# Performance work log

Measured on AMD Instinct MI355X. Metric: run time of the kernel, lower is better.

Reference implementation:

```python
import jax, jax.numpy as jnp
import numpy as np

B, S, N = 1, 128, 256
D_MSA, D_PAIR, D_HID = 256, 128, 32
EPS = 1e-3
LN_EPS = 1e-5


def _layer_norm(x, w, b):
    mu = jnp.mean(x, axis=-1, keepdims=True)
    var = jnp.mean(jnp.square(x - mu), axis=-1, keepdims=True)
    return (x - mu) * jax.lax.rsqrt(var + LN_EPS) * w + b


def setup_inputs() -> dict:
    key = jax.random.key(0)
    ks = jax.random.split(key, 8)
    sc = lambda fan_in: (1.0 / fan_in) ** 0.5
    return {
        "m": jax.random.normal(ks[0], (B, S, N, D_MSA), dtype=jnp.float32),
        "mask": jnp.ones((B, S, N), dtype=jnp.float32),
        "ln_w": jnp.ones((D_MSA,), dtype=jnp.float32),
        "ln_b": jnp.zeros((D_MSA,), dtype=jnp.float32),
        "w1": jax.random.normal(ks[1], (D_HID, D_MSA), dtype=jnp.float32) * sc(D_MSA),
        "b1": jnp.zeros((D_HID,), dtype=jnp.float32),
        "w2": jax.random.normal(ks[2], (D_HID, D_MSA), dtype=jnp.float32) * sc(D_MSA),
        "b2": jnp.zeros((D_HID,), dtype=jnp.float32),
        "w_out": jax.random.normal(ks[3], (D_PAIR, D_HID * D_HID), dtype=jnp.float32) * sc(D_HID * D_HID),
        "b_out": jnp.zeros((D_PAIR,), dtype=jnp.float32),
        "ln_out_w": jnp.ones((D_PAIR,), dtype=jnp.float32),
        "ln_out_b": jnp.zeros((D_PAIR,), dtype=jnp.float32),
        "wz": jax.random.normal(ks[4], (D_PAIR, D_PAIR), dtype=jnp.float32) * sc(D_PAIR),
        "bz": jnp.zeros((D_PAIR,), dtype=jnp.float32),
    }


def reference(m, mask, ln_w, ln_b, w1, b1, w2, b2, w_out, b_out, ln_out_w, ln_out_b, wz, bz):
    # m: [B, S, N, d_msa], mask: [B, S, N]
    x = _layer_norm(m, ln_w, ln_b)
    n_res = mask.shape[-1]
    mk = mask[..., None] * (n_res ** -0.5)          # [B, S, N, 1] (layer_norm_out branch)
    a = (jnp.einsum('bsnd,hd->bsnh', x, w1) + b1) * mk
    b_ = (jnp.einsum('bsnd,hd->bsnh', x, w2) + b2) * mk
    a = jnp.swapaxes(a, -2, -3)                      # [B, N, S, h]
    b_ = jnp.swapaxes(b_, -2, -3)                    # [B, N, S, h]
    outer = jnp.einsum('bisc,bjse->bijce', a, b_)    # [B, N, N, h, h]
    outer = outer.reshape(outer.shape[:-2] + (-1,))  # [B, N, N, h*h]
    z = jnp.einsum('bijk,pk->bijp', outer, w_out) + b_out  # [B, N, N, d_pair]
    norm = jnp.einsum('bsi,bsj->bij', mk[..., 0], mk[..., 0])[..., None]
    z = z / (EPS + norm)
    z = jax.nn.gelu(z, approximate=False)
    z = _layer_norm(z, ln_out_w, ln_out_b)
    z = jnp.einsum('bijp,qp->bijq', z, wz) + bz
    return z
```

## Files before the change

### kernel.cpp

```cpp
#include <hip/hip_runtime.h>
#include <hip/hip_bf16.h>
#include <math.h>

#define EPSC 1e-3f

typedef __attribute__((ext_vector_type(8)))  short  short8;
typedef __attribute__((ext_vector_type(4)))  float  float4v;
typedef __attribute__((ext_vector_type(16))) float  float16v;

static __device__ __forceinline__ unsigned short f2bf(float f) {
    union { float f; unsigned u; } x; x.f = f;
    unsigned r = x.u + 0x7FFFu + ((x.u >> 16) & 1u);
    return (unsigned short)(r >> 16);
}
static __device__ __forceinline__ unsigned pk_bf16(float lo, float hi) {
    union { __hip_bfloat162 h; unsigned u; } cv;
    cv.h = __float22bfloat162_rn(make_float2(lo, hi));
    return cv.u;
}
static __device__ __forceinline__ float4v mfma16(short8 a, short8 b, float4v c) {
    return __builtin_amdgcn_mfma_f32_16x16x32_bf16(a, b, c, 0, 0, 0);
}
static __device__ __forceinline__ float16v mfma32(short8 a, short8 b, float16v c) {
    return __builtin_amdgcn_mfma_f32_32x32x16_bf16(a, b, c, 0, 0, 0);
}

#define OFF_NORM 0ull
#define OFF_AT   262144ull
#define OFF_BT   2359296ull
#define OFF_WOF  4456448ull
#define OFF_WZF  4718592ull
#define OFF_W12  4751360ull

__global__ __launch_bounds__(256) void k_pre(
    const float* __restrict__ m, const float* __restrict__ mask,
    const float* __restrict__ ln_w, const float* __restrict__ ln_b,
    const float* __restrict__ w1, const float* __restrict__ b1,
    const float* __restrict__ w2, const float* __restrict__ b2,
    const float* __restrict__ w_out, const float* __restrict__ wz,
    unsigned short* __restrict__ aT, unsigned short* __restrict__ bT,
    unsigned short* __restrict__ wobF, unsigned short* __restrict__ wzF,
    const unsigned short* __restrict__ w12F_in,
    unsigned short* __restrict__ w12F,
    float* __restrict__ normw)
{
    __shared__ unsigned short xs[64 * 264];
    __shared__ unsigned short tr[64 * 76];
    __shared__ float mkl[64];
    __shared__ float b12[64];
    int t = threadIdx.x;
    int b = blockIdx.x;

    if (b >= 1152) {
        int i = b - 1152, j = t;
        float acc = 0.f;
#pragma unroll 8
        for (int s = 0; s < 128; ++s)
            acc += mask[s * 256 + i] * mask[s * 256 + j];
        normw[i * 256 + j] = acc * (1.0f / 256.0f);
        return;
    }
    if (b >= 512) {
        int idx = (b - 512) * 256 + t;
        if (idx < 131072) {
            int j = idx & 7, lane = (idx >> 3) & 63, k16 = (idx >> 9) & 63, pw = idx >> 15;
            int p = pw * 32 + (lane & 31);
            int k = k16 * 16 + (lane >> 5) * 8 + j;
            wobF[idx] = f2bf(w_out[p * 1024 + k]);
        } else if (idx < 147456) {
            int q = idx - 131072;
            int j = q & 7, lane = (q >> 3) & 63, kk = (q >> 9) & 3, w = q >> 11;
            int p = w * 16 + (lane & 15);
            int k = kk * 32 + (lane >> 4) * 8 + j;
            wzF[q] = f2bf(wz[p * 128 + k]);
        } else if (idx < 163840) {
            int q = idx - 147456;
            int j = q & 7, lane = (q >> 3) & 63, ht = (q >> 9) & 3, kk = q >> 11;
            int h = ht * 16 + (lane & 15);
            int d = kk * 32 + (lane >> 4) * 8 + j;
            w12F[q] = f2bf(h < 32 ? w1[h * 256 + d] : w2[(h - 32) * 256 + d]);
        }
        return;
    }

    int w = t >> 6, lane = t & 63;
    int g = lane >> 4, l15 = lane & 15;
    int n0 = (b & 31) * 8, s0 = (b >> 5) * 8;

    if (t < 64) {
        b12[t] = (t < 32) ? b1[t] : b2[t - 32];
        mkl[t] = mask[(s0 + (t >> 3)) * 256 + n0 + (t & 7)] * 0.0625f;
    }

    float4 lwv = *(const float4*)(ln_w + lane * 4);
    float4 lbv = *(const float4*)(ln_b + lane * 4);

#pragma unroll 4
    for (int i = 0; i < 16; ++i) {
        int r = w * 16 + i;
        size_t gr = (size_t)(s0 + (r >> 3)) * 256 + n0 + (r & 7);
        float4 v = *(const float4*)(m + gr * 256 + lane * 4);
        float sum = v.x + v.y + v.z + v.w;
        float sq = v.x * v.x + v.y * v.y + v.z * v.z + v.w * v.w;
#pragma unroll
        for (int off = 32; off > 0; off >>= 1) {
            sum += __shfl_xor(sum, off, 64);
            sq  += __shfl_xor(sq, off, 64);
        }
        float mu = sum * (1.f / 256.f);
        float rstd = rsqrtf(sq * (1.f / 256.f) - mu * mu + 1e-5f);
        uint2 u;
        u.x = pk_bf16((v.x - mu) * rstd * lwv.x + lbv.x, (v.y - mu) * rstd * lwv.y + lbv.y);
        u.y = pk_bf16((v.z - mu) * rstd * lwv.z + lbv.z, (v.w - mu) * rstd * lwv.w + lbv.w);
        *(uint2*)(xs + r * 264 + lane * 4) = u;
    }
    __syncthreads();

    float4v zf4 = {0.f, 0.f, 0.f, 0.f};
    float4v acc[4]; acc[0] = zf4; acc[1] = zf4; acc[2] = zf4; acc[3] = zf4;
#pragma unroll
    for (int kk = 0; kk < 8; ++kk) {
        short8 af = *(const short8*)(xs + (w * 16 + l15) * 264 + kk * 32 + g * 8);
#pragma unroll
        for (int ht = 0; ht < 4; ++ht) {
            short8 bfr = *(const short8*)(w12F_in + ((size_t)(kk * 4 + ht) * 64 + lane) * 8);
            acc[ht] = mfma16(af, bfr, acc[ht]);
        }
    }
#pragma unroll
    for (int ht = 0; ht < 4; ++ht) {
        int h = ht * 16 + l15;
        float bias = b12[h];
        int rbase = w * 16 + g * 4;
        uint2 u;
        u.x = pk_bf16((acc[ht][0] + bias) * mkl[rbase + 0], (acc[ht][1] + bias) * mkl[rbase + 1]);
        u.y = pk_bf16((acc[ht][2] + bias) * mkl[rbase + 2], (acc[ht][3] + bias) * mkl[rbase + 3]);
        *(uint2*)(tr + h * 76 + rbase) = u;
    }
    __syncthreads();

#pragma unroll
    for (int it = 0; it < 2; ++it) {
        int q = t + it * 256;
        int h = q >> 3, n_l = q & 7;
        unsigned short vv[8];
#pragma unroll
        for (int s_l = 0; s_l < 8; ++s_l)
            vv[s_l] = tr[h * 76 + s_l * 8 + n_l];
        uint4 u;
        u.x = (unsigned)vv[0] | ((unsigned)vv[1] << 16);
        u.y = (unsigned)vv[2] | ((unsigned)vv[3] << 16);
        u.z = (unsigned)vv[4] | ((unsigned)vv[5] << 16);
        u.w = (unsigned)vv[6] | ((unsigned)vv[7] << 16);
        unsigned short* dst = ((h < 32) ? aT : bT) + ((size_t)(n0 + n_l) * 32 + (h & 31)) * 128 + s0;
        *(uint4*)dst = u;
    }
}

__global__ __launch_bounds__(512, 2) void k2_fused(
    const unsigned short* __restrict__ aT, const unsigned short* __restrict__ bT,
    const unsigned short* __restrict__ wobF, const unsigned short* __restrict__ wzF,
    const float* __restrict__ b_out, const float* __restrict__ normw,
    const float* __restrict__ ln_ow, const float* __restrict__ ln_ob,
    const float* __restrict__ bz, float* __restrict__ out)
{
    __shared__ char smem[131072];
    unsigned* s32 = (unsigned*)smem;
    unsigned* oL = (unsigned*)smem;
    float* zL = (float*)smem;
    unsigned short* lnL = (unsigned short*)(smem + 36864);

    int t = threadIdx.x;
    int w = t >> 6, lane = t & 63;
    int g = lane >> 4, l15 = lane & 15;
    int bj = blockIdx.x, bi = blockIdx.y;
    int wn = w & 1, wm = w >> 1;

    {
        const uint4* Agv = (const uint4*)(aT + (size_t)bi * 256 * 128);
        const uint4* Bgv = (const uint4*)(bT + (size_t)bj * 256 * 128);
#pragma unroll
        for (int it = 0; it < 8; ++it) {
            int q = t + it * 512;
            int row = q >> 4, col4 = (q & 15) * 4;
            int dcol = col4 ^ ((row & 7) << 2);
            *(uint4*)(s32 + row * 64 + dcol) = Agv[q];
            *(uint4*)(s32 + 16384 + row * 64 + dcol) = Bgv[q];
        }
    }
    __syncthreads();

    float4v zf4 = {0.f, 0.f, 0.f, 0.f};
    float4v acc[4][8];
#pragma unroll
    for (int fm = 0; fm < 4; ++fm)
#pragma unroll
        for (int fn = 0; fn < 8; ++fn) acc[fm][fn] = zf4;

    {
        int sw = (l15 & 7) << 2;
#pragma unroll
        for (int kk = 0; kk < 4; ++kk) {
            int col = (kk * 16 + g * 4) ^ sw;
            short8 af[4], bf[8];
#pragma unroll
            for (int fm = 0; fm < 4; ++fm) {
                int row = wm * 64 + fm * 16 + l15;
                af[fm] = *(const short8*)((const char*)(s32 + row * 64 + col));
            }
#pragma unroll
            for (int fn = 0; fn < 8; ++fn) {
                int row = wn * 128 + fn * 16 + l15;
                bf[fn] = *(const short8*)((const char*)(s32 + 16384 + row * 64 + col));
            }
#pragma unroll
            for (int fm = 0; fm < 4; ++fm)
#pragma unroll
                for (int fn = 0; fn < 8; ++fn)
                    acc[fm][fn] = mfma16(bf[fn], af[fm], acc[fm][fn]);
        }
    }
    __syncthreads();

#pragma unroll
    for (int fm = 0; fm < 4; ++fm) {
#pragma unroll
        for (int fn = 0; fn < 8; ++fn) {
            int pair = (wm * 2 + (fm >> 1)) * 8 + wn * 4 + (fn >> 1);
            int c = (fm & 1) * 16 + l15;
            int o = (fn & 1) * 8 + 2 * g;
            int off = c * 16 + o;
            int dw = pair * 512 + (off ^ ((((pair & 7) ^ (off >> 6)) & 7) << 2));
            float4v a4 = acc[fm][fn];
            uint2 u;
            u.x = pk_bf16(a4[0], a4[1]);
            u.y = pk_bf16(a4[2], a4[3]);
            *(uint2*)(oL + dw) = u;
        }
    }
    __syncthreads();

    {
        int pw = w & 3, ph = w >> 2;
        int l31 = lane & 31, h2 = lane >> 5;
        int pairR = ph * 32 + l31;
        int prebase = pairR * 512;
        int psw = (pairR & 7);
        float16v acc32 = {0.f};
        const unsigned short* wbase = wobF + (size_t)pw * 32768;
#pragma unroll 8
        for (int k16 = 0; k16 < 64; ++k16) {
            int off = k16 * 8 + h2 * 4;
            int dw = prebase + (off ^ (((psw ^ (off >> 6)) & 7) << 2));
            short8 a2 = *(const short8*)((const char*)(oL + dw));
            short8 b2 = *(const short8*)(wbase + ((size_t)(k16 * 64 + lane)) * 8);
            acc32 = mfma32(a2, b2, acc32);
        }
        __syncthreads();
#pragma unroll
        for (int reg = 0; reg < 16; ++reg) {
            int prow = ph * 32 + (reg & 3) + 8 * (reg >> 2) + 4 * h2;
            zL[prow * 132 + pw * 32 + l31] = acc32[reg];
        }
    }
    __syncthreads();

    {
        const float4 loA = *(const float4*)(ln_ow + l15 * 8);
        const float4 loB = *(const float4*)(ln_ow + l15 * 8 + 4);
        const float4 lbA = *(const float4*)(ln_ob + l15 * 8);
        const float4 lbB = *(const float4*)(ln_ob + l15 * 8 + 4);
        const float4 boA = *(const float4*)(b_out + l15 * 8);
        const float4 boB = *(const float4*)(b_out + l15 * 8 + 4);
        float lw8[8] = {loA.x, loA.y, loA.z, loA.w, loB.x, loB.y, loB.z, loB.w};
        float lb8[8] = {lbA.x, lbA.y, lbA.z, lbA.w, lbB.x, lbB.y, lbB.z, lbB.w};
        float bo8[8] = {boA.x, boA.y, boA.z, boA.w, boB.x, boB.y, boB.z, boB.w};
#pragma unroll
        for (int it = 0; it < 2; ++it) {
            int pair = w * 8 + it * 4 + g;
            int iG = bi * 8 + (pair >> 3), jG = bj * 8 + (pair & 7);
            float inv = 1.0f / (EPSC + normw[iG * 256 + jG]);
            float4v z0 = *(const float4v*)(zL + pair * 132 + l15 * 8);
            float4v z1 = *(const float4v*)(zL + pair * 132 + l15 * 8 + 4);
            float vals[8];
            float sum = 0.f, sq = 0.f;
#pragma unroll
            for (int e2 = 0; e2 < 8; ++e2) {
                float v = ((e2 < 4) ? z0[e2] : z1[e2 - 4]) + bo8[e2];
                v *= inv;
                v = 0.5f * v * (1.0f + erff(v * 0.70710678118654752f));
                vals[e2] = v; sum += v; sq += v * v;
            }
#pragma unroll
            for (int mm = 1; mm <= 8; mm <<= 1) {
                sum += __shfl_xor(sum, mm);
                sq  += __shfl_xor(sq, mm);
            }
            float mu = sum * (1.0f / 128.0f);
            float rstd = rsqrtf(sq * (1.0f / 128.0f) - mu * mu + 1e-5f);
            uint4 upk;
            upk.x = pk_bf16((vals[0] - mu) * rstd * lw8[0] + lb8[0],
                            (vals[1] - mu) * rstd * lw8[1] + lb8[1]);
            upk.y = pk_bf16((vals[2] - mu) * rstd * lw8[2] + lb8[2],
                            (vals[3] - mu) * rstd * lw8[3] + lb8[3]);
            upk.z = pk_bf16((vals[4] - mu) * rstd * lw8[4] + lb8[4],
                            (vals[5] - mu) * rstd * lw8[5] + lb8[5]);
            upk.w = pk_bf16((vals[6] - mu) * rstd * lw8[6] + lb8[6],
                            (vals[7] - mu) * rstd * lw8[7] + lb8[7]);
            *(uint4*)(lnL + pair * 136 + l15 * 8) = upk;
        }
    }
    __syncthreads();

    {
        float4v acc3[4]; acc3[0] = zf4; acc3[1] = zf4; acc3[2] = zf4; acc3[3] = zf4;
#pragma unroll
        for (int kk = 0; kk < 4; ++kk) {
            short8 bfw = *(const short8*)(wzF + ((size_t)(w * 4 + kk) * 64 + lane) * 8);
#pragma unroll
            for (int fr = 0; fr < 4; ++fr) {
                short8 af3 = *(const short8*)(lnL + (fr * 16 + l15) * 136 + kk * 32 + g * 8);
                acc3[fr] = mfma16(af3, bfw, acc3[fr]);
            }
        }
        float bzq = bz[w * 16 + l15];
#pragma unroll
        for (int fr = 0; fr < 4; ++fr) {
#pragma unroll
            for (int r = 0; r < 4; ++r) {
                int pair = fr * 16 + g * 4 + r;
                int row = (bi * 8 + (pair >> 3)) * 256 + bj * 8 + (pair & 7);
                out[(size_t)row * 128 + w * 16 + l15] = acc3[fr][r] + bzq;
            }
        }
    }
}

extern "C" void kernel_launch(void* const* d_in, const int* in_sizes, int n_in,
                              void* d_out, int out_size, void* d_ws, size_t ws_size,
                              hipStream_t stream) {
    const float* m      = (const float*)d_in[0];
    const float* mask   = (const float*)d_in[1];
    const float* ln_w   = (const float*)d_in[2];
    const float* ln_b   = (const float*)d_in[3];
    const float* w1     = (const float*)d_in[4];
    const float* b1     = (const float*)d_in[5];
    const float* w2     = (const float*)d_in[6];
    const float* b2     = (const float*)d_in[7];
    const float* w_out  = (const float*)d_in[8];
    const float* b_out  = (const float*)d_in[9];
    const float* ln_ow  = (const float*)d_in[10];
    const float* ln_ob  = (const float*)d_in[11];
    const float* wz     = (const float*)d_in[12];
    const float* bz     = (const float*)d_in[13];
    float* out = (float*)d_out;
    char*  ws  = (char*)d_ws;

    float* normw          = (float*)(ws + OFF_NORM);
    unsigned short* aTb   = (unsigned short*)(ws + OFF_AT);
    unsigned short* bTb   = (unsigned short*)(ws + OFF_BT);
    unsigned short* wobF  = (unsigned short*)(ws + OFF_WOF);
    unsigned short* wzF   = (unsigned short*)(ws + OFF_WZF);
    unsigned short* w12F  = (unsigned short*)(ws + OFF_W12);

    {
        struct L {
            static __global__ void __launch_bounds__(256) cvt12(
                const float* __restrict__ w1, const float* __restrict__ w2,
                unsigned short* __restrict__ w12F) {
                int q = blockIdx.x * 256 + threadIdx.x;
                int j = q & 7, lane = (q >> 3) & 63, ht = (q >> 9) & 3, kk = q >> 11;
                int h = ht * 16 + (lane & 15);
                int d = kk * 32 + (lane >> 4) * 8 + j;
                w12F[q] = f2bf(h < 32 ? w1[h * 256 + d] : w2[(h - 32) * 256 + d]);
            }
        };
        L::cvt12<<<dim3(64), dim3(256), 0, stream>>>(w1, w2, w12F);
    }
    k_pre<<<dim3(1408), dim3(256), 0, stream>>>(m, mask, ln_w, ln_b, w1, b1, w2, b2,
                                                w_out, wz, aTb, bTb, wobF, wzF,
                                                w12F, w12F, normw);
    k2_fused<<<dim3(32, 32), dim3(512), 0, stream>>>(aTb, bTb, wobF, wzF, b_out, normw,
                                                     ln_ow, ln_ob, bz, out);
}
```

Measured before the change: 166.9 us.

## Split K in the w_out projection, pre-swizzle aT/bT, and widen LayerNorm row loads

In the fused pair kernel, each warp now computes two 32-row output tiles over half of K and shares each w_out fragment between them. The two K-halves go to separate LDS buffers and are summed during the GELU/LayerNorm epilogue, which halves weight-fragment global loads per MFMA. The pre-kernel now writes aT/bT already in the XOR-swizzled tile layout, so the fused kernel copies them into LDS linearly. The MSA LayerNorm now reads four rows per warp pass with a 16-lane reduction, and the xs row pitch is padded to 266. The cost is more LDS for the split accumulators and an extra add in the epilogue.

```diff
diff --git a/kernel.cpp b/kernel.cpp
--- a/kernel.cpp
+++ b/kernel.cpp
@@ -44,7 +44,7 @@
     unsigned short* __restrict__ w12F,
     float* __restrict__ normw)
 {
-    __shared__ unsigned short xs[64 * 264];
+    __shared__ unsigned short xs[64 * 266];
     __shared__ unsigned short tr[64 * 76];
     __shared__ float mkl[64];
     __shared__ float b12[64];
@@ -63,9 +63,10 @@
     if (b >= 512) {
         int idx = (b - 512) * 256 + t;
         if (idx < 131072) {
-            int j = idx & 7, lane = (idx >> 3) & 63, k16 = (idx >> 9) & 63, pw = idx >> 15;
+            int j = idx & 7, lane = (idx >> 3) & 63, k16 = (idx >> 9) & 31;
+            int kh = (idx >> 14) & 1, pw = (idx >> 15) & 3;
             int p = pw * 32 + (lane & 31);
-            int k = k16 * 16 + (lane >> 5) * 8 + j;
+            int k = kh * 512 + k16 * 16 + (lane >> 5) * 8 + j;
             wobF[idx] = f2bf(w_out[p * 1024 + k]);
         } else if (idx < 147456) {
             int q = idx - 131072;
@@ -85,6 +86,7 @@
 
     int w = t >> 6, lane = t & 63;
     int g = lane >> 4, l15 = lane & 15;
+    int rr = lane >> 4, l16 = lane & 15;
     int n0 = (b & 31) * 8, s0 = (b >> 5) * 8;
 
     if (t < 64) {
@@ -92,27 +94,43 @@
         mkl[t] = mask[(s0 + (t >> 3)) * 256 + n0 + (t & 7)] * 0.0625f;
     }
 
-    float4 lwv = *(const float4*)(ln_w + lane * 4);
-    float4 lbv = *(const float4*)(ln_b + lane * 4);
-
-#pragma unroll 4
-    for (int i = 0; i < 16; ++i) {
-        int r = w * 16 + i;
-        size_t gr = (size_t)(s0 + (r >> 3)) * 256 + n0 + (r & 7);
-        float4 v = *(const float4*)(m + gr * 256 + lane * 4);
-        float sum = v.x + v.y + v.z + v.w;
-        float sq = v.x * v.x + v.y * v.y + v.z * v.z + v.w * v.w;
-#pragma unroll
-        for (int off = 32; off > 0; off >>= 1) {
-            sum += __shfl_xor(sum, off, 64);
-            sq  += __shfl_xor(sq, off, 64);
+    float4 lw4[4], lb4[4];
+#pragma unroll
+    for (int q = 0; q < 4; ++q) {
+        lw4[q] = *(const float4*)(ln_w + q * 64 + l16 * 4);
+        lb4[q] = *(const float4*)(ln_b + q * 64 + l16 * 4);
+    }
+
+#pragma unroll
+    for (int pass = 0; pass < 4; ++pass) {
+        int r = w * 16 + pass * 4 + rr;
+        const float* src = m + ((size_t)(s0 + (r >> 3)) * 256 + n0 + (r & 7)) * 256;
+        float4 v[4];
+#pragma unroll
+        for (int q = 0; q < 4; ++q)
+            v[q] = *(const float4*)(src + q * 64 + l16 * 4);
+        float sum = 0.f, sq = 0.f;
+#pragma unroll
+        for (int q = 0; q < 4; ++q) {
+            sum += v[q].x + v[q].y + v[q].z + v[q].w;
+            sq  += v[q].x * v[q].x + v[q].y * v[q].y + v[q].z * v[q].z + v[q].w * v[q].w;
+        }
+#pragma unroll
+        for (int mm = 1; mm <= 8; mm <<= 1) {
+            sum += __shfl_xor(sum, mm);
+            sq  += __shfl_xor(sq, mm);
         }
         float mu = sum * (1.f / 256.f);
         float rstd = rsqrtf(sq * (1.f / 256.f) - mu * mu + 1e-5f);
-        uint2 u;
-        u.x = pk_bf16((v.x - mu) * rstd * lwv.x + lbv.x, (v.y - mu) * rstd * lwv.y + lbv.y);
-        u.y = pk_bf16((v.z - mu) * rstd * lwv.z + lbv.z, (v.w - mu) * rstd * lwv.w + lbv.w);
-        *(uint2*)(xs + r * 264 + lane * 4) = u;
+#pragma unroll
+        for (int q = 0; q < 4; ++q) {
+            uint2 u;
+            u.x = pk_bf16((v[q].x - mu) * rstd * lw4[q].x + lb4[q].x,
+                          (v[q].y - mu) * rstd * lw4[q].y + lb4[q].y);
+            u.y = pk_bf16((v[q].z - mu) * rstd * lw4[q].z + lb4[q].z,
+                          (v[q].w - mu) * rstd * lw4[q].w + lb4[q].w);
+            *(uint2*)(xs + r * 266 + q * 64 + l16 * 4) = u;
+        }
     }
     __syncthreads();
 
@@ -120,7 +138,7 @@
     float4v acc[4]; acc[0] = zf4; acc[1] = zf4; acc[2] = zf4; acc[3] = zf4;
 #pragma unroll
     for (int kk = 0; kk < 8; ++kk) {
-        short8 af = *(const short8*)(xs + (w * 16 + l15) * 264 + kk * 32 + g * 8);
+        short8 af = *(const short8*)(xs + (w * 16 + l15) * 266 + kk * 32 + g * 8);
 #pragma unroll
         for (int ht = 0; ht < 4; ++ht) {
             short8 bfr = *(const short8*)(w12F_in + ((size_t)(kk * 4 + ht) * 64 + lane) * 8);
@@ -152,7 +170,10 @@
         u.y = (unsigned)vv[2] | ((unsigned)vv[3] << 16);
         u.z = (unsigned)vv[4] | ((unsigned)vv[5] << 16);
         u.w = (unsigned)vv[6] | ((unsigned)vv[7] << 16);
-        unsigned short* dst = ((h < 32) ? aT : bT) + ((size_t)(n0 + n_l) * 32 + (h & 31)) * 128 + s0;
+        int row = n_l * 32 + (h & 31);
+        int dwcol = (s0 >> 1) ^ ((row & 7) << 2);
+        unsigned short* dst = ((h < 32) ? aT : bT)
+            + (size_t)(n0 >> 3) * 32768 + row * 128 + dwcol * 2;
         *(uint4*)dst = u;
     }
 }
@@ -167,8 +188,9 @@
     __shared__ char smem[131072];
     unsigned* s32 = (unsigned*)smem;
     unsigned* oL = (unsigned*)smem;
-    float* zL = (float*)smem;
-    unsigned short* lnL = (unsigned short*)(smem + 36864);
+    float* zA = (float*)smem;
+    float* zB = (float*)(smem + 33792);
+    unsigned short* lnL = (unsigned short*)(smem + 67584);
 
     int t = threadIdx.x;
     int w = t >> 6, lane = t & 63;
@@ -177,15 +199,13 @@
     int wn = w & 1, wm = w >> 1;
 
     {
-        const uint4* Agv = (const uint4*)(aT + (size_t)bi * 256 * 128);
-        const uint4* Bgv = (const uint4*)(bT + (size_t)bj * 256 * 128);
+        const uint4* Agv = (const uint4*)(aT + (size_t)bi * 32768);
+        const uint4* Bgv = (const uint4*)(bT + (size_t)bj * 32768);
 #pragma unroll
         for (int it = 0; it < 8; ++it) {
             int q = t + it * 512;
-            int row = q >> 4, col4 = (q & 15) * 4;
-            int dcol = col4 ^ ((row & 7) << 2);
-            *(uint4*)(s32 + row * 64 + dcol) = Agv[q];
-            *(uint4*)(s32 + 16384 + row * 64 + dcol) = Bgv[q];
+            *(uint4*)(s32 + q * 4) = Agv[q];
+            *(uint4*)(s32 + 16384 + q * 4) = Bgv[q];
         }
     }
     __syncthreads();
@@ -241,26 +261,29 @@
     __syncthreads();
 
     {
-        int pw = w & 3, ph = w >> 2;
+        int pw = w >> 1, kh = w & 1;
         int l31 = lane & 31, h2 = lane >> 5;
-        int pairR = ph * 32 + l31;
-        int prebase = pairR * 512;
-        int psw = (pairR & 7);
-        float16v acc32 = {0.f};
-        const unsigned short* wbase = wobF + (size_t)pw * 32768;
+        float16v accA = {0.f};
+        float16v accB = {0.f};
+        const unsigned short* wbase = wobF + (size_t)w * 16384;
 #pragma unroll 8
-        for (int k16 = 0; k16 < 64; ++k16) {
-            int off = k16 * 8 + h2 * 4;
-            int dw = prebase + (off ^ (((psw ^ (off >> 6)) & 7) << 2));
-            short8 a2 = *(const short8*)((const char*)(oL + dw));
-            short8 b2 = *(const short8*)(wbase + ((size_t)(k16 * 64 + lane)) * 8);
-            acc32 = mfma32(a2, b2, acc32);
+        for (int k16 = 0; k16 < 32; ++k16) {
+            int kg = kh * 32 + k16;
+            int off = kg * 8 + h2 * 4;
+            int dws = off ^ ((((l31 & 7) ^ (off >> 6)) & 7) << 2);
+            short8 b2 = *(const short8*)(wbase + (size_t)(k16 * 64 + lane) * 8);
+            short8 aA = *(const short8*)(oL + l31 * 512 + dws);
+            short8 aB = *(const short8*)(oL + (32 + l31) * 512 + dws);
+            accA = mfma32(aA, b2, accA);
+            accB = mfma32(aB, b2, accB);
         }
         __syncthreads();
+        float* zdst = kh ? zB : zA;
 #pragma unroll
         for (int reg = 0; reg < 16; ++reg) {
-            int prow = ph * 32 + (reg & 3) + 8 * (reg >> 2) + 4 * h2;
-            zL[prow * 132 + pw * 32 + l31] = acc32[reg];
+            int pr = (reg & 3) + 8 * (reg >> 2) + 4 * h2;
+            zdst[pr * 132 + pw * 32 + l31] = accA[reg];
+            zdst[(32 + pr) * 132 + pw * 32 + l31] = accB[reg];
         }
     }
     __syncthreads();
@@ -280,13 +303,15 @@
             int pair = w * 8 + it * 4 + g;
             int iG = bi * 8 + (pair >> 3), jG = bj * 8 + (pair & 7);
             float inv = 1.0f / (EPSC + normw[iG * 256 + jG]);
-            float4v z0 = *(const float4v*)(zL + pair * 132 + l15 * 8);
-            float4v z1 = *(const float4v*)(zL + pair * 132 + l15 * 8 + 4);
+            float4v zA0 = *(const float4v*)(zA + pair * 132 + l15 * 8);
+            float4v zA1 = *(const float4v*)(zA + pair * 132 + l15 * 8 + 4);
+            float4v zB0 = *(const float4v*)(zB + pair * 132 + l15 * 8);
+            float4v zB1 = *(const float4v*)(zB + pair * 132 + l15 * 8 + 4);
             float vals[8];
             float sum = 0.f, sq = 0.f;
 #pragma unroll
             for (int e2 = 0; e2 < 8; ++e2) {
-                float v = ((e2 < 4) ? z0[e2] : z1[e2 - 4]) + bo8[e2];
+                float v = ((e2 < 4) ? (zA0[e2] + zB0[e2]) : (zA1[e2 - 4] + zB1[e2 - 4])) + bo8[e2];
                 v *= inv;
                 v = 0.5f * v * (1.0f + erff(v * 0.70710678118654752f));
                 vals[e2] = v; sum += v; sq += v * v;
```

Result: no change. 166.2 us (-0.4%).
